# Kernel tuning notes

Hardware: AMD Instinct MI355X
Metric: run time of the kernel (lower is better)

Reference implementation:

```python
import jax, jax.numpy as jnp
import numpy as np

N_NODES = 100000
HEADS = 4
HEAD_DIM = 32  # hidden_channels // heads
NEG_SLOPE = 0.2


def gat_layer(x, W, a_src, a_dst, b, src, dst):
    # x: [N, Fin], W: [Fin, H*C], a_src/a_dst: [H, C], b: [H*C]
    N = x.shape[0]
    h = (x @ W).reshape(N, HEADS, HEAD_DIM)            # [N, H, C]
    alpha_s = jnp.einsum('nhc,hc->nh', h, a_src)       # [N, H]
    alpha_d = jnp.einsum('nhc,hc->nh', h, a_dst)       # [N, H]
    e = jax.nn.leaky_relu(alpha_s[src] + alpha_d[dst], NEG_SLOPE)  # [E, H]
    # segment softmax over edges grouped by destination node
    e_max = jax.ops.segment_max(e, dst, num_segments=N)           # [N, H]
    ex = jnp.exp(e - e_max[dst])                                   # [E, H]
    denom = jax.ops.segment_sum(ex, dst, num_segments=N)          # [N, H]
    alpha = ex / denom[dst]                                        # [E, H]
    msg = h[src] * alpha[:, :, None]                               # [E, H, C]
    out = jax.ops.segment_sum(msg, dst, num_segments=N)           # [N, H, C]
    return out.reshape(N, HEADS * HEAD_DIM) + b


def setup_inputs() -> dict:
    key = jax.random.key(0)
    ks = jax.random.split(key, 10)
    Fin, H, C = 128, HEADS, HEAD_DIM
    x = jax.random.normal(ks[0], (N_NODES, Fin), dtype=jnp.float32)
    edge_index = jax.random.randint(ks[1], (2, 1000000), 0, N_NODES, dtype=jnp.int64)
    s = 1.0 / np.sqrt(Fin)
    W1 = jax.random.normal(ks[2], (Fin, H * C), dtype=jnp.float32) * s
    a_src1 = jax.random.normal(ks[3], (H, C), dtype=jnp.float32) * 0.1
    a_dst1 = jax.random.normal(ks[4], (H, C), dtype=jnp.float32) * 0.1
    b1 = jnp.zeros((H * C,), dtype=jnp.float32)
    s2 = 1.0 / np.sqrt(H * C)
    W2 = jax.random.normal(ks[5], (H * C, H * C), dtype=jnp.float32) * s2
    a_src2 = jax.random.normal(ks[6], (H, C), dtype=jnp.float32) * 0.1
    a_dst2 = jax.random.normal(ks[7], (H, C), dtype=jnp.float32) * 0.1
    b2 = jnp.zeros((H * C,), dtype=jnp.float32)
    return {"x": x, "edge_index": edge_index, "W1": W1, "a_src1": a_src1,
            "a_dst1": a_dst1, "b1": b1, "W2": W2, "a_src2": a_src2,
            "a_dst2": a_dst2, "b2": b2}


def reference(x, edge_index, W1, a_src1, a_dst1, b1, W2, a_src2, a_dst2, b2):
    N = x.shape[0]
    # add self-loops (PyG add_self_loops=True)
    loop = jnp.arange(N, dtype=edge_index.dtype)
    src = jnp.concatenate([edge_index[0], loop])
    dst = jnp.concatenate([edge_index[1], loop])
    h = gat_layer(x, W1, a_src1, a_dst1, b1, src, dst)
    h = jax.nn.elu(h)
    h = gat_layer(h, W2, a_src2, a_dst2, b2, src, dst)
    h = jax.nn.elu(h)
    return h
```

## Files before the change

### kernel.cpp

```cpp
#include <hip/hip_runtime.h>
#include <math.h>

#define NHEADS 4
#define HDIM 32
#define F 128
#define ACH 8192
#define LOG2E 1.44269504088896340736f

typedef __attribute__((ext_vector_type(8))) short bf16x8;
typedef __attribute__((ext_vector_type(4))) float f32x4;
typedef __attribute__((ext_vector_type(4))) unsigned u32x4;

__device__ __forceinline__ float lrelu(float v) { return v > 0.f ? v : 0.2f * v; }

__device__ __forceinline__ unsigned short cvt_bf16(float f) {
    unsigned u = __float_as_uint(f);
    u += 0x7fffu + ((u >> 16) & 1u);
    return (unsigned short)(u >> 16);
}

__global__ void k_packW2(const float* __restrict__ W1, const float* __restrict__ as1,
                         const float* __restrict__ ad1, const float* __restrict__ W2,
                         const float* __restrict__ as2, const float* __restrict__ ad2,
                         short* __restrict__ Wb) {
    int idx = blockIdx.x * 256 + threadIdx.x;
    if (idx >= 2 * 36 * 512) return;
    int half = idx >= 36 * 512;
    const float* W     = half ? W2 : W1;
    const float* a_src = half ? as2 : as1;
    const float* a_dst = half ? ad2 : ad1;
    int r = idx - half * 36 * 512;
    int j    = r & 7;
    int lane = (r >> 3) & 63;
    int frag = r >> 9;
    int kk = frag / 9, ct = frag % 9;
    int k = kk * 32 + (lane >> 4) * 8 + j;
    int col = lane & 15;
    float val;
    if (ct < 8) {
        val = W[k * F + ct * 16 + col];
    } else if (col < 8) {
        int head = col & 3;
        const float* av = (col < 4) ? a_src : a_dst;
        float sum = 0.f;
        #pragma unroll 8
        for (int c = 0; c < HDIM; ++c)
            sum += W[k * F + head * HDIM + c] * av[head * HDIM + c];
        val = sum;
    } else {
        val = 0.f;
    }
    Wb[idx] = (short)cvt_bf16(val);
}

template<bool ABF16>
__global__ __launch_bounds__(256) void k_gemm_mfma(
    const void* __restrict__ xv, const short* __restrict__ Wb,
    unsigned short* __restrict__ hbf, float* __restrict__ as_out,
    float* __restrict__ ad_out, int N)
{
    const int wid  = threadIdx.x >> 6;
    const int lane = threadIdx.x & 63;
    const int rowbase = blockIdx.x * 64 + wid * 16;
    const int row  = rowbase + (lane & 15);
    const int rowc = min(row, N - 1);
    const int col = lane & 15;

    f32x4 acc[9] = {};
    #pragma unroll
    for (int kk = 0; kk < 4; ++kk) {
        bf16x8 a;
        if constexpr (ABF16) {
            const unsigned short* xr =
                (const unsigned short*)xv + (size_t)rowc * F + (lane >> 4) * 8;
            a = *(const bf16x8*)(xr + kk * 32);
        } else {
            const float* xr = (const float*)xv + (size_t)rowc * F + (lane >> 4) * 8;
            float4 xa = *(const float4*)(xr + kk * 32);
            float4 xb = *(const float4*)(xr + kk * 32 + 4);
            a[0] = cvt_bf16(xa.x); a[1] = cvt_bf16(xa.y);
            a[2] = cvt_bf16(xa.z); a[3] = cvt_bf16(xa.w);
            a[4] = cvt_bf16(xb.x); a[5] = cvt_bf16(xb.y);
            a[6] = cvt_bf16(xb.z); a[7] = cvt_bf16(xb.w);
        }
        const bf16x8* bp = (const bf16x8*)(Wb + (size_t)(kk * 9) * 512 + lane * 8);
        #pragma unroll
        for (int ct = 0; ct < 9; ++ct) {
            bf16x8 b = bp[ct * 64];
            acc[ct] = __builtin_amdgcn_mfma_f32_16x16x32_bf16(a, b, acc[ct], 0, 0, 0);
        }
    }

    const int r0 = rowbase + (lane >> 4) * 4;
    #pragma unroll
    for (int i = 0; i < 4; ++i) {
        int r = r0 + i;
        if (r < N) {
            #pragma unroll
            for (int ct = 0; ct < 8; ++ct)
                __builtin_nontemporal_store(cvt_bf16(acc[ct][i]),
                                            &hbf[(size_t)r * F + ct * 16 + col]);
            if (col < 4)       as_out[r * NHEADS + col]     = acc[8][i] * LOG2E;
            else if (col < 8)  ad_out[r * NHEADS + col - 4] = acc[8][i] * LOG2E;
        }
    }
}


__global__ __launch_bounds__(512) void k_bhist(
    const int* __restrict__ src, const int* __restrict__ dst,
    int* __restrict__ bha, int nbuc, int E, int TOT)
{
    __shared__ int hist[512];
    int t = threadIdx.x;
    hist[t] = 0;
    __syncthreads();
    int base = blockIdx.x * ACH;
    for (int k = 0; k < ACH / 512; ++k) {
        int i = base + k * 512 + t;
        if (i < TOT) {
            int d = (i < E) ? dst[i] : (i - E);
            atomicAdd(&hist[d >> 8], 1);
        }
    }
    __syncthreads();
    if (t < nbuc) bha[(size_t)blockIdx.x * nbuc + t] = hist[t];
}

__global__ __launch_bounds__(512) void k_bscan(
    int* __restrict__ bha, int* __restrict__ bbase, int* __restrict__ bh,
    int nbuc, int nab, int nbh)
{
    int t = threadIdx.x;
    for (int i = t; i < nbh; i += 512) bh[i] = 0;
    int run = 0;
    if (t < nbuc) {
        int j = 0;
        for (; j + 8 <= nab; j += 8) {
            int v[8];
            #pragma unroll
            for (int u = 0; u < 8; ++u) v[u] = bha[(size_t)(j + u) * nbuc + t];
            #pragma unroll
            for (int u = 0; u < 8; ++u) { bha[(size_t)(j + u) * nbuc + t] = run; run += v[u]; }
        }
        for (; j < nab; ++j) {
            int v = bha[(size_t)j * nbuc + t];
            bha[(size_t)j * nbuc + t] = run; run += v;
        }
    }
    __shared__ int sh[512];
    sh[t] = run;
    __syncthreads();
    for (int off = 1; off < 512; off <<= 1) {
        int u = (t >= off) ? sh[t - off] : 0;
        __syncthreads();
        sh[t] += u;
        __syncthreads();
    }
    if (t < nbuc) {
        bbase[t] = sh[t] - run;
        if (t == nbuc - 1) bbase[nbuc] = sh[t];
    }
}

__global__ __launch_bounds__(512) void k_bscatter(
    const int* __restrict__ src, const int* __restrict__ dst,
    const int* __restrict__ bha, const int* __restrict__ bbase,
    unsigned* __restrict__ epack, int nbuc, int E, int TOT)
{
    __shared__ int cur[512];
    int t = threadIdx.x;
    cur[t] = (t < nbuc) ? (bha[(size_t)blockIdx.x * nbuc + t] + bbase[t]) : 0;
    __syncthreads();
    int base = blockIdx.x * ACH;
    for (int k = 0; k < ACH / 512; ++k) {
        int i = base + k * 512 + t;
        if (i < TOT) {
            int s, d;
            if (i < E) { s = src[i]; d = dst[i]; } else { s = d = i - E; }
            int pos = atomicAdd(&cur[d >> 8], 1);
            epack[pos] = ((unsigned)s << 8) | (unsigned)(d & 255);
        }
    }
}

__global__ __launch_bounds__(256) void k_bfinal(
    const unsigned* __restrict__ epack, const int* __restrict__ bbase,
    int* __restrict__ deg, int* __restrict__ rowptr, int* __restrict__ ssrc,
    int* __restrict__ bh, int N, int nbuc)
{
    __shared__ int hist[256];
    __shared__ int sh[256];
    __shared__ int cur[256];
    int t = threadIdx.x;
    hist[t] = 0;
    __syncthreads();
    int s0 = bbase[blockIdx.x], s1 = bbase[blockIdx.x + 1];
    for (int i = s0 + t; i < s1; i += 256)
        atomicAdd(&hist[epack[i] & 255u], 1);
    __syncthreads();
    int h = hist[t];
    sh[t] = h;
    __syncthreads();
    for (int off = 1; off < 256; off <<= 1) {
        int u = (t >= off) ? sh[t - off] : 0;
        __syncthreads();
        sh[t] += u;
        __syncthreads();
    }
    int node = blockIdx.x * 256 + t;
    int excl = s0 + sh[t] - h;
    cur[t] = excl;
    if (node < N) {
        deg[node] = h;
        rowptr[node] = excl;
        atomicAdd(&bh[(blockIdx.x >> 2) * 256 + min(h, 255)], 1);
    }
    if (node == 0) rowptr[N] = bbase[nbuc];
    __syncthreads();
    for (int i = s0 + t; i < s1; i += 256) {
        unsigned p = epack[i];
        int pos = atomicAdd(&cur[p & 255u], 1);
        ssrc[pos] = (int)(p >> 8);
    }
}

__global__ __launch_bounds__(256) void k_sort_off(int* __restrict__ bh, int nb)
{
    int t = threadIdx.x;
    int run = 0;
    int j = 0;
    for (; j + 8 <= nb; j += 8) {
        int v[8];
        #pragma unroll
        for (int u = 0; u < 8; ++u) v[u] = bh[(j + u) * 256 + t];
        #pragma unroll
        for (int u = 0; u < 8; ++u) { bh[(j + u) * 256 + t] = run; run += v[u]; }
    }
    for (; j < nb; ++j) {
        int v = bh[j * 256 + t];
        bh[j * 256 + t] = run;
        run += v;
    }
    __shared__ int sh[256];
    int tot = run;
    sh[t] = tot;
    __syncthreads();
    for (int off = 1; off < 256; off <<= 1) {
        int u = (t >= off) ? sh[t - off] : 0;
        __syncthreads();
        sh[t] += u;
        __syncthreads();
    }
    int total = sh[255];
    int bucket_base = total - sh[t];
    for (int j2 = 0; j2 < nb; ++j2)
        bh[j2 * 256 + t] += bucket_base;
}

__global__ __launch_bounds__(256) void k_sort_scatter(
    const int* __restrict__ deg, const int* __restrict__ bh,
    const int* __restrict__ rowptr, int4* __restrict__ ninfo, int N)
{
    __shared__ int cur[256];
    int t = threadIdx.x;
    cur[t] = bh[blockIdx.x * 256 + t];
    __syncthreads();
    int base = blockIdx.x * 1024;
    #pragma unroll
    for (int g = 0; g < 4; ++g) {
        int i = base + g * 256 + t;
        if (i < N) {
            int pos = atomicAdd(&cur[min(deg[i], 255)], 1);
            ninfo[pos] = make_int4(rowptr[i], rowptr[i + 1], i, 0);
        }
    }
}

template<bool OUTBF16>
__global__ __launch_bounds__(256) void k_aggregate(
    const int4* __restrict__ ninfo, const int* __restrict__ ssrc,
    const float* __restrict__ as, const float* __restrict__ ad,
    const unsigned short* __restrict__ hbf, const float* __restrict__ bias,
    void* __restrict__ outv, int N)
{
    int gi = (blockIdx.x * 256 + threadIdx.x) >> 4;
    if (gi >= N) return;
    const int4 ni   = ninfo[gi];
    const int start = ni.x, end = ni.y, node = ni.z;
    const int l16   = threadIdx.x & 15;
    const int hb    = l16 >> 2;
    const int c0    = l16 * 8;
    const float adB = ad[node * NHEADS + hb];

    float a0=0.f,a1=0.f,a2=0.f,a3=0.f,a4=0.f,a5=0.f,a6=0.f,a7=0.f;
    float dacc = 0.f;
    for (int base = start; base < end; base += 8) {
        int   sj[8];
        float fj[8];
        uint4 hj[8];
        #pragma unroll
        for (int j = 0; j < 8; ++j)
            sj[j] = ssrc[min(base + j, end - 1)];
        #pragma unroll
        for (int j = 0; j < 8; ++j)
            fj[j] = as[sj[j] * NHEADS + hb];
        #pragma unroll
        for (int j = 0; j < 8; ++j)
            hj[j] = *(const uint4*)(hbf + (size_t)sj[j] * F + c0);
        #pragma unroll
        for (int j = 0; j < 8; ++j) {
            float ex = (base + j < end) ? exp2f(lrelu(fj[j] + adB)) : 0.f;
            dacc += ex;
            a0 = fmaf(ex, __uint_as_float(hj[j].x << 16),         a0);
            a1 = fmaf(ex, __uint_as_float(hj[j].x & 0xffff0000u), a1);
            a2 = fmaf(ex, __uint_as_float(hj[j].y << 16),         a2);
            a3 = fmaf(ex, __uint_as_float(hj[j].y & 0xffff0000u), a3);
            a4 = fmaf(ex, __uint_as_float(hj[j].z << 16),         a4);
            a5 = fmaf(ex, __uint_as_float(hj[j].z & 0xffff0000u), a5);
            a6 = fmaf(ex, __uint_as_float(hj[j].w << 16),         a6);
            a7 = fmaf(ex, __uint_as_float(hj[j].w & 0xffff0000u), a7);
        }
    }
    float inv = 1.f / dacc;
    float v[8] = {a0,a1,a2,a3,a4,a5,a6,a7};
    #pragma unroll
    for (int k = 0; k < 8; ++k) {
        float t = v[k] * inv + bias[c0 + k];
        v[k] = t > 0.f ? t : expm1f(t);
    }
    if (OUTBF16) {
        u32x4 o;
        o.x = (unsigned)cvt_bf16(v[0]) | ((unsigned)cvt_bf16(v[1]) << 16);
        o.y = (unsigned)cvt_bf16(v[2]) | ((unsigned)cvt_bf16(v[3]) << 16);
        o.z = (unsigned)cvt_bf16(v[4]) | ((unsigned)cvt_bf16(v[5]) << 16);
        o.w = (unsigned)cvt_bf16(v[6]) | ((unsigned)cvt_bf16(v[7]) << 16);
        __builtin_nontemporal_store(o,
            (u32x4*)((unsigned short*)outv + (size_t)node * F + c0));
    } else {
        f32x4 o0 = {v[0], v[1], v[2], v[3]};
        f32x4 o1 = {v[4], v[5], v[6], v[7]};
        float* op = (float*)outv + (size_t)node * F + c0;
        __builtin_nontemporal_store(o0, (f32x4*)op);
        __builtin_nontemporal_store(o1, (f32x4*)(op + 4));
    }
}

extern "C" void kernel_launch(void* const* d_in, const int* in_sizes, int n_in,
                              void* d_out, int out_size, void* d_ws, size_t ws_size,
                              hipStream_t stream)
{
    const float* x      = (const float*)d_in[0];
    const int*   eidx   = (const int*)d_in[1];
    const float* W1     = (const float*)d_in[2];
    const float* a_src1 = (const float*)d_in[3];
    const float* a_dst1 = (const float*)d_in[4];
    const float* b1     = (const float*)d_in[5];
    const float* W2     = (const float*)d_in[6];
    const float* a_src2 = (const float*)d_in[7];
    const float* a_dst2 = (const float*)d_in[8];
    const float* b2     = (const float*)d_in[9];

    const int N = in_sizes[0] / F;
    const int E = in_sizes[1] / 2;
    const int TOT = E + N;
    const int* src = eidx;
    const int* dst = eidx + E;

    const int nbuc = (N + 255) / 256;
    const int nab  = (TOT + ACH - 1) / ACH;
    const int nb   = (N + 1023) / 1024;

    unsigned* epack = (unsigned*)d_ws;
    unsigned short* hbf    = (unsigned short*)(epack + TOT);
    unsigned short* out1bf = hbf + (size_t)N * F;
    float* as = (float*)(out1bf + (size_t)N * F);
    float* ad = as + (size_t)N * NHEADS;
    int* deg    = (int*)(ad + (size_t)N * NHEADS);
    int* rowptr = deg + N;
    int* ssrc   = rowptr + N + 1;
    int4* ninfo = (int4*)(((uintptr_t)(ssrc + TOT) + 15) & ~(uintptr_t)15);
    int* bh     = (int*)(ninfo + N);
    int* bha    = bh + (size_t)nb * 256;
    int* btot   = bha + (size_t)nab * nbuc;
    int* bbase  = btot + nbuc;
    short* Wb1  = (short*)(((uintptr_t)(bbase + nbuc + 1) + 15) & ~(uintptr_t)15);

    const int gemmBlocks = (N + 63) / 64;
    const int aggBlocks  = (N + 15) / 16;

    k_packW2<<<144, 256, 0, stream>>>(W1, a_src1, a_dst1, W2, a_src2, a_dst2, Wb1);
    short* Wb2 = Wb1 + 36 * 512;

    k_bhist<<<nab, 512, 0, stream>>>(src, dst, bha, nbuc, E, TOT);
    k_bscan<<<1, 512, 0, stream>>>(bha, bbase, bh, nbuc, nab, nb * 256);
    k_bscatter<<<nab, 512, 0, stream>>>(src, dst, bha, bbase, epack, nbuc, E, TOT);
    k_bfinal<<<nbuc, 256, 0, stream>>>(epack, bbase, deg, rowptr, ssrc, bh, N, nbuc);

    k_sort_off<<<1, 256, 0, stream>>>(bh, nb);
    k_sort_scatter<<<nb, 256, 0, stream>>>(deg, bh, rowptr, ninfo, N);

    k_gemm_mfma<false><<<gemmBlocks, 256, 0, stream>>>(x, Wb1, hbf, as, ad, N);
    k_aggregate<true><<<aggBlocks, 256, 0, stream>>>(ninfo, ssrc, as, ad, hbf, b1, out1bf, N);

    k_gemm_mfma<true><<<gemmBlocks, 256, 0, stream>>>(out1bf, Wb2, hbf, as, ad, N);
    k_aggregate<false><<<aggBlocks, 256, 0, stream>>>(ninfo, ssrc, as, ad, hbf, b2, d_out, N);
}
```

Before: 240.6 us.

## Fuse graph CSR build and weight packing into one cooperative kernel

Replaces seven separate preprocessing launches (weight packing, bucket histogram, scan, scatter, per-bucket finalize, degree-sort offset and scatter) with a single cooperative kernel that uses grid-wide syncs between phases. The aim is to remove launch overhead and idle gaps between small kernels. In exchange, single-block scan phases now stall the whole grid at each barrier, and phases that previously ran with more blocks are now looped over nab blocks, so there is less parallelism in some stages.

```diff
diff --git a/kernel.cpp b/kernel.cpp
--- a/kernel.cpp
+++ b/kernel.cpp
@@ -1,5 +1,8 @@
 #include <hip/hip_runtime.h>
+#include <hip/hip_cooperative_groups.h>
 #include <math.h>
+
+namespace cg = cooperative_groups;
 
 #define NHEADS 4
 #define HDIM 32
@@ -17,40 +20,6 @@
     unsigned u = __float_as_uint(f);
     u += 0x7fffu + ((u >> 16) & 1u);
     return (unsigned short)(u >> 16);
-}
-
-__global__ void k_packW2(const float* __restrict__ W1, const float* __restrict__ as1,
-                         const float* __restrict__ ad1, const float* __restrict__ W2,
-                         const float* __restrict__ as2, const float* __restrict__ ad2,
-                         short* __restrict__ Wb) {
-    int idx = blockIdx.x * 256 + threadIdx.x;
-    if (idx >= 2 * 36 * 512) return;
-    int half = idx >= 36 * 512;
-    const float* W     = half ? W2 : W1;
-    const float* a_src = half ? as2 : as1;
-    const float* a_dst = half ? ad2 : ad1;
-    int r = idx - half * 36 * 512;
-    int j    = r & 7;
-    int lane = (r >> 3) & 63;
-    int frag = r >> 9;
-    int kk = frag / 9, ct = frag % 9;
-    int k = kk * 32 + (lane >> 4) * 8 + j;
-    int col = lane & 15;
-    float val;
-    if (ct < 8) {
-        val = W[k * F + ct * 16 + col];
-    } else if (col < 8) {
-        int head = col & 3;
-        const float* av = (col < 4) ? a_src : a_dst;
-        float sum = 0.f;
-        #pragma unroll 8
-        for (int c = 0; c < HDIM; ++c)
-            sum += W[k * F + head * HDIM + c] * av[head * HDIM + c];
-        val = sum;
-    } else {
-        val = 0.f;
-    }
-    Wb[idx] = (short)cvt_bf16(val);
 }
 
 template<bool ABF16>
@@ -106,174 +75,208 @@
     }
 }
 
-
-__global__ __launch_bounds__(512) void k_bhist(
-    const int* __restrict__ src, const int* __restrict__ dst,
-    int* __restrict__ bha, int nbuc, int E, int TOT)
+struct PrepArgs {
+    const int* src; const int* dst;
+    const float *W1, *as1, *ad1, *W2, *as2, *ad2;
+    short* Wb;
+    int* bha; int* bbase; int* bh;
+    unsigned* epack; int* deg; int* rowptr; int* ssrc;
+    int4* ninfo;
+    int N, E, TOT, nbuc, nab, nb;
+};
+
+__global__ __launch_bounds__(512) void k_prep(PrepArgs a)
 {
-    __shared__ int hist[512];
-    int t = threadIdx.x;
-    hist[t] = 0;
+    cg::grid_group grid = cg::this_grid();
+    __shared__ int lds0[512];
+    __shared__ int lhist[256];
+    __shared__ int lsh[256];
+    __shared__ int lcur[256];
+    const int t = threadIdx.x;
+    const int b = blockIdx.x;
+    const int nbuc = a.nbuc, nab = a.nab, nb = a.nb, N = a.N, E = a.E, TOT = a.TOT;
+
+    lds0[t] = 0;
     __syncthreads();
-    int base = blockIdx.x * ACH;
-    for (int k = 0; k < ACH / 512; ++k) {
-        int i = base + k * 512 + t;
-        if (i < TOT) {
-            int d = (i < E) ? dst[i] : (i - E);
-            atomicAdd(&hist[d >> 8], 1);
-        }
+    {
+        int base = b * ACH;
+        for (int k = 0; k < ACH / 512; ++k) {
+            int i = base + k * 512 + t;
+            if (i < TOT) {
+                int d = (i < E) ? a.dst[i] : (i - E);
+                atomicAdd(&lds0[d >> 8], 1);
+            }
+        }
+    }
+    for (int idx = b * 512 + t; idx < 2 * 36 * 512; idx += (int)gridDim.x * 512) {
+        int half = idx >= 36 * 512;
+        const float* W     = half ? a.W2 : a.W1;
+        const float* a_src = half ? a.as2 : a.as1;
+        const float* a_dst = half ? a.ad2 : a.ad1;
+        int r = idx - half * 36 * 512;
+        int j    = r & 7;
+        int lane = (r >> 3) & 63;
+        int frag = r >> 9;
+        int kk = frag / 9, ct = frag % 9;
+        int k = kk * 32 + (lane >> 4) * 8 + j;
+        int col = lane & 15;
+        float val;
+        if (ct < 8) {
+            val = W[k * F + ct * 16 + col];
+        } else if (col < 8) {
+            int head = col & 3;
+            const float* av = (col < 4) ? a_src : a_dst;
+            float sum = 0.f;
+            #pragma unroll 8
+            for (int c = 0; c < HDIM; ++c)
+                sum += W[k * F + head * HDIM + c] * av[head * HDIM + c];
+            val = sum;
+        } else {
+            val = 0.f;
+        }
+        a.Wb[idx] = (short)cvt_bf16(val);
     }
     __syncthreads();
-    if (t < nbuc) bha[(size_t)blockIdx.x * nbuc + t] = hist[t];
-}
-
-__global__ __launch_bounds__(512) void k_bscan(
-    int* __restrict__ bha, int* __restrict__ bbase, int* __restrict__ bh,
-    int nbuc, int nab, int nbh)
-{
-    int t = threadIdx.x;
-    for (int i = t; i < nbh; i += 512) bh[i] = 0;
-    int run = 0;
-    if (t < nbuc) {
-        int j = 0;
-        for (; j + 8 <= nab; j += 8) {
-            int v[8];
-            #pragma unroll
-            for (int u = 0; u < 8; ++u) v[u] = bha[(size_t)(j + u) * nbuc + t];
-            #pragma unroll
-            for (int u = 0; u < 8; ++u) { bha[(size_t)(j + u) * nbuc + t] = run; run += v[u]; }
-        }
-        for (; j < nab; ++j) {
-            int v = bha[(size_t)j * nbuc + t];
-            bha[(size_t)j * nbuc + t] = run; run += v;
-        }
-    }
-    __shared__ int sh[512];
-    sh[t] = run;
+    if (t < nbuc) a.bha[(size_t)b * nbuc + t] = lds0[t];
+    __threadfence();
+    grid.sync();
+
+    if (b == 0) {
+        for (int i = t; i < nb * 256; i += 512) a.bh[i] = 0;
+        int run = 0;
+        if (t < nbuc) {
+            int j = 0;
+            for (; j + 8 <= nab; j += 8) {
+                int v[8];
+                #pragma unroll
+                for (int u = 0; u < 8; ++u) v[u] = a.bha[(size_t)(j + u) * nbuc + t];
+                #pragma unroll
+                for (int u = 0; u < 8; ++u) { a.bha[(size_t)(j + u) * nbuc + t] = run; run += v[u]; }
+            }
+            for (; j < nab; ++j) {
+                int v = a.bha[(size_t)j * nbuc + t];
+                a.bha[(size_t)j * nbuc + t] = run; run += v;
+            }
+        }
+        lds0[t] = run;
+        __syncthreads();
+        for (int off = 1; off < 512; off <<= 1) {
+            int u = (t >= off) ? lds0[t - off] : 0;
+            __syncthreads();
+            lds0[t] += u;
+            __syncthreads();
+        }
+        if (t < nbuc) {
+            a.bbase[t] = lds0[t] - run;
+            if (t == nbuc - 1) a.bbase[nbuc] = lds0[t];
+        }
+    }
+    __threadfence();
+    grid.sync();
+
+    lds0[t] = (t < nbuc) ? (a.bha[(size_t)b * nbuc + t] + a.bbase[t]) : 0;
     __syncthreads();
-    for (int off = 1; off < 512; off <<= 1) {
-        int u = (t >= off) ? sh[t - off] : 0;
-        __syncthreads();
-        sh[t] += u;
-        __syncthreads();
-    }
-    if (t < nbuc) {
-        bbase[t] = sh[t] - run;
-        if (t == nbuc - 1) bbase[nbuc] = sh[t];
-    }
-}
-
-__global__ __launch_bounds__(512) void k_bscatter(
-    const int* __restrict__ src, const int* __restrict__ dst,
-    const int* __restrict__ bha, const int* __restrict__ bbase,
-    unsigned* __restrict__ epack, int nbuc, int E, int TOT)
-{
-    __shared__ int cur[512];
-    int t = threadIdx.x;
-    cur[t] = (t < nbuc) ? (bha[(size_t)blockIdx.x * nbuc + t] + bbase[t]) : 0;
-    __syncthreads();
-    int base = blockIdx.x * ACH;
-    for (int k = 0; k < ACH / 512; ++k) {
-        int i = base + k * 512 + t;
-        if (i < TOT) {
-            int s, d;
-            if (i < E) { s = src[i]; d = dst[i]; } else { s = d = i - E; }
-            int pos = atomicAdd(&cur[d >> 8], 1);
-            epack[pos] = ((unsigned)s << 8) | (unsigned)(d & 255);
-        }
-    }
-}
-
-__global__ __launch_bounds__(256) void k_bfinal(
-    const unsigned* __restrict__ epack, const int* __restrict__ bbase,
-    int* __restrict__ deg, int* __restrict__ rowptr, int* __restrict__ ssrc,
-    int* __restrict__ bh, int N, int nbuc)
-{
-    __shared__ int hist[256];
-    __shared__ int sh[256];
-    __shared__ int cur[256];
-    int t = threadIdx.x;
-    hist[t] = 0;
-    __syncthreads();
-    int s0 = bbase[blockIdx.x], s1 = bbase[blockIdx.x + 1];
-    for (int i = s0 + t; i < s1; i += 256)
-        atomicAdd(&hist[epack[i] & 255u], 1);
-    __syncthreads();
-    int h = hist[t];
-    sh[t] = h;
-    __syncthreads();
-    for (int off = 1; off < 256; off <<= 1) {
-        int u = (t >= off) ? sh[t - off] : 0;
-        __syncthreads();
-        sh[t] += u;
-        __syncthreads();
-    }
-    int node = blockIdx.x * 256 + t;
-    int excl = s0 + sh[t] - h;
-    cur[t] = excl;
-    if (node < N) {
-        deg[node] = h;
-        rowptr[node] = excl;
-        atomicAdd(&bh[(blockIdx.x >> 2) * 256 + min(h, 255)], 1);
-    }
-    if (node == 0) rowptr[N] = bbase[nbuc];
-    __syncthreads();
-    for (int i = s0 + t; i < s1; i += 256) {
-        unsigned p = epack[i];
-        int pos = atomicAdd(&cur[p & 255u], 1);
-        ssrc[pos] = (int)(p >> 8);
-    }
-}
-
-__global__ __launch_bounds__(256) void k_sort_off(int* __restrict__ bh, int nb)
-{
-    int t = threadIdx.x;
-    int run = 0;
-    int j = 0;
-    for (; j + 8 <= nb; j += 8) {
-        int v[8];
-        #pragma unroll
-        for (int u = 0; u < 8; ++u) v[u] = bh[(j + u) * 256 + t];
-        #pragma unroll
-        for (int u = 0; u < 8; ++u) { bh[(j + u) * 256 + t] = run; run += v[u]; }
-    }
-    for (; j < nb; ++j) {
-        int v = bh[j * 256 + t];
-        bh[j * 256 + t] = run;
-        run += v;
-    }
-    __shared__ int sh[256];
-    int tot = run;
-    sh[t] = tot;
-    __syncthreads();
-    for (int off = 1; off < 256; off <<= 1) {
-        int u = (t >= off) ? sh[t - off] : 0;
-        __syncthreads();
-        sh[t] += u;
-        __syncthreads();
-    }
-    int total = sh[255];
-    int bucket_base = total - sh[t];
-    for (int j2 = 0; j2 < nb; ++j2)
-        bh[j2 * 256 + t] += bucket_base;
-}
-
-__global__ __launch_bounds__(256) void k_sort_scatter(
-    const int* __restrict__ deg, const int* __restrict__ bh,
-    const int* __restrict__ rowptr, int4* __restrict__ ninfo, int N)
-{
-    __shared__ int cur[256];
-    int t = threadIdx.x;
-    cur[t] = bh[blockIdx.x * 256 + t];
-    __syncthreads();
-    int base = blockIdx.x * 1024;
-    #pragma unroll
-    for (int g = 0; g < 4; ++g) {
-        int i = base + g * 256 + t;
-        if (i < N) {
-            int pos = atomicAdd(&cur[min(deg[i], 255)], 1);
-            ninfo[pos] = make_int4(rowptr[i], rowptr[i + 1], i, 0);
-        }
+    {
+        int base = b * ACH;
+        for (int k = 0; k < ACH / 512; ++k) {
+            int i = base + k * 512 + t;
+            if (i < TOT) {
+                int s, d;
+                if (i < E) { s = a.src[i]; d = a.dst[i]; } else { s = d = i - E; }
+                int pos = atomicAdd(&lds0[d >> 8], 1);
+                a.epack[pos] = ((unsigned)s << 8) | (unsigned)(d & 255);
+            }
+        }
+    }
+    __threadfence();
+    grid.sync();
+
+    for (int bk = b; bk < nbuc; bk += (int)gridDim.x) {
+        if (t < 256) lhist[t] = 0;
+        __syncthreads();
+        int s0 = a.bbase[bk], s1 = a.bbase[bk + 1];
+        for (int i = s0 + t; i < s1; i += 512)
+            atomicAdd(&lhist[a.epack[i] & 255u], 1);
+        __syncthreads();
+        int h = 0;
+        if (t < 256) { h = lhist[t]; lsh[t] = h; }
+        __syncthreads();
+        for (int off = 1; off < 256; off <<= 1) {
+            int u = (t >= off && t < 256) ? lsh[t - off] : 0;
+            __syncthreads();
+            if (t < 256) lsh[t] += u;
+            __syncthreads();
+        }
+        if (t < 256) {
+            int node = bk * 256 + t;
+            int excl = s0 + lsh[t] - h;
+            lcur[t] = excl;
+            if (node < N) {
+                a.deg[node] = h;
+                a.rowptr[node] = excl;
+                atomicAdd(&a.bh[(bk >> 2) * 256 + min(h, 255)], 1);
+            }
+            if (node == 0) a.rowptr[N] = a.bbase[nbuc];
+        }
+        __syncthreads();
+        for (int i = s0 + t; i < s1; i += 512) {
+            unsigned p = a.epack[i];
+            int pos = atomicAdd(&lcur[p & 255u], 1);
+            a.ssrc[pos] = (int)(p >> 8);
+        }
+        __syncthreads();
+    }
+    __threadfence();
+    grid.sync();
+
+    if (b == 0) {
+        int run = 0;
+        if (t < 256) {
+            int j = 0;
+            for (; j + 8 <= nb; j += 8) {
+                int v[8];
+                #pragma unroll
+                for (int u = 0; u < 8; ++u) v[u] = a.bh[(j + u) * 256 + t];
+                #pragma unroll
+                for (int u = 0; u < 8; ++u) { a.bh[(j + u) * 256 + t] = run; run += v[u]; }
+            }
+            for (; j < nb; ++j) {
+                int v = a.bh[j * 256 + t];
+                a.bh[j * 256 + t] = run;
+                run += v;
+            }
+            lsh[t] = run;
+        }
+        __syncthreads();
+        for (int off = 1; off < 256; off <<= 1) {
+            int u = (t >= off && t < 256) ? lsh[t - off] : 0;
+            __syncthreads();
+            if (t < 256) lsh[t] += u;
+            __syncthreads();
+        }
+        int total = lsh[255];
+        if (t < 256) {
+            int bucket_base = total - lsh[t];
+            for (int j2 = 0; j2 < nb; ++j2)
+                a.bh[j2 * 256 + t] += bucket_base;
+        }
+    }
+    __threadfence();
+    grid.sync();
+
+    for (int cb = b; cb < nb; cb += (int)gridDim.x) {
+        if (t < 256) lcur[t] = a.bh[cb * 256 + t];
+        __syncthreads();
+        int base = cb * 1024;
+        #pragma unroll
+        for (int g = 0; g < 2; ++g) {
+            int i = base + g * 512 + t;
+            if (i < N) {
+                int pos = atomicAdd(&lcur[min(a.deg[i], 255)], 1);
+                a.ninfo[pos] = make_int4(a.rowptr[i], a.rowptr[i + 1], i, 0);
+            }
+        }
+        __syncthreads();
     }
 }
 
@@ -385,20 +388,23 @@
     int* btot   = bha + (size_t)nab * nbuc;
     int* bbase  = btot + nbuc;
     short* Wb1  = (short*)(((uintptr_t)(bbase + nbuc + 1) + 15) & ~(uintptr_t)15);
+    short* Wb2  = Wb1 + 36 * 512;
 
     const int gemmBlocks = (N + 63) / 64;
     const int aggBlocks  = (N + 15) / 16;
 
-    k_packW2<<<144, 256, 0, stream>>>(W1, a_src1, a_dst1, W2, a_src2, a_dst2, Wb1);
-    short* Wb2 = Wb1 + 36 * 512;
-
-    k_bhist<<<nab, 512, 0, stream>>>(src, dst, bha, nbuc, E, TOT);
-    k_bscan<<<1, 512, 0, stream>>>(bha, bbase, bh, nbuc, nab, nb * 256);
-    k_bscatter<<<nab, 512, 0, stream>>>(src, dst, bha, bbase, epack, nbuc, E, TOT);
-    k_bfinal<<<nbuc, 256, 0, stream>>>(epack, bbase, deg, rowptr, ssrc, bh, N, nbuc);
-
-    k_sort_off<<<1, 256, 0, stream>>>(bh, nb);
-    k_sort_scatter<<<nb, 256, 0, stream>>>(deg, bh, rowptr, ninfo, N);
+    PrepArgs pa;
+    pa.src = src; pa.dst = dst;
+    pa.W1 = W1; pa.as1 = a_src1; pa.ad1 = a_dst1;
+    pa.W2 = W2; pa.as2 = a_src2; pa.ad2 = a_dst2;
+    pa.Wb = Wb1;
+    pa.bha = bha; pa.bbase = bbase; pa.bh = bh;
+    pa.epack = epack; pa.deg = deg; pa.rowptr = rowptr; pa.ssrc = ssrc;
+    pa.ninfo = ninfo;
+    pa.N = N; pa.E = E; pa.TOT = TOT; pa.nbuc = nbuc; pa.nab = nab; pa.nb = nb;
+    void* kargs[] = { &pa };
+    (void)hipLaunchCooperativeKernel((void*)k_prep, dim3(nab), dim3(512),
+                                     kargs, 0, stream);
 
     k_gemm_mfma<false><<<gemmBlocks, 256, 0, stream>>>(x, Wb1, hbf, as, ad, N);
     k_aggregate<true><<<aggBlocks, 256, 0, stream>>>(ninfo, ssrc, as, ad, hbf, b1, out1bf, N);
```

Result: slower. 455.0 us (+89.1%).
